# Performance work log

Measured on AMD Instinct MI355X. Metric: run time of the kernel, lower is better.

Reference implementation:

```python
import jax, jax.numpy as jnp
import numpy as np

B, L, V, E, H, S = 64, 128, 100000, 300, 400, 50
HD = H // 2
START_IDX, END_IDX = S - 2, S - 1


def setup_inputs():
    key = jax.random.key(0)
    ks = jax.random.split(key, 10)
    words = jax.random.randint(ks[0], (B, L), 0, V)
    word_seq_lens = jnp.full((B,), L, dtype=jnp.int32)
    masks = jnp.ones((B, L), dtype=bool)
    tags = jax.random.randint(ks[1], (B, L), 0, S - 2)
    emb_table = jax.random.normal(ks[2], (V, E), dtype=jnp.float32) * 0.1
    lw = lambda k, shp: jax.random.normal(k, shp, dtype=jnp.float32) * 0.05
    w_ih_f = lw(ks[3], (4 * HD, E)); w_hh_f = lw(ks[4], (4 * HD, HD)); b_f = jnp.zeros((4 * HD,), jnp.float32)
    w_ih_b = lw(ks[5], (4 * HD, E)); w_hh_b = lw(ks[6], (4 * HD, HD)); b_b = jnp.zeros((4 * HD,), jnp.float32)
    W_tag = lw(ks[7], (S, H)); b_tag = jnp.zeros((S,), jnp.float32)
    transition = jax.random.normal(ks[8], (S, S), dtype=jnp.float32)
    transition = transition.at[:, START_IDX].set(-10000.0).at[END_IDX, :].set(-10000.0)
    return dict(words=words, word_seq_lens=word_seq_lens, masks=masks, tags=tags,
                emb_table=emb_table, w_ih_f=w_ih_f, w_hh_f=w_hh_f, b_f=b_f,
                w_ih_b=w_ih_b, w_hh_b=w_hh_b, b_b=b_b, W_tag=W_tag, b_tag=b_tag,
                transition=transition)


def _lstm_dir(x, w_ih, w_hh, b, reverse):
    # x: (B, L, D) -> (B, L, HD). PyTorch gate order: i, f, g, o.
    bsz = x.shape[0]
    xg = jnp.einsum('bld,gd->blg', x, w_ih) + b  # precompute input projections

    def step(carry, xt):
        h, c = carry
        g = xt + h @ w_hh.T
        i, f, gg, o = jnp.split(g, 4, axis=-1)
        c = jax.nn.sigmoid(f) * c + jax.nn.sigmoid(i) * jnp.tanh(gg)
        h = jax.nn.sigmoid(o) * jnp.tanh(c)
        return (h, c), h

    init = (jnp.zeros((bsz, HD), x.dtype), jnp.zeros((bsz, HD), x.dtype))
    _, hs = jax.lax.scan(step, init, jnp.swapaxes(xg, 0, 1), reverse=reverse)
    return jnp.swapaxes(hs, 0, 1)


def _forward_nll(words, word_seq_lens, masks, tags, emb_table,
                 w_ih_f, w_hh_f, b_f, w_ih_b, w_hh_b, b_b, W_tag, b_tag, transition):
    word_emb = emb_table[words]                              # (B, L, E); dropout = identity (eval)
    h_f = _lstm_dir(word_emb, w_ih_f, w_hh_f, b_f, reverse=False)
    h_b = _lstm_dir(word_emb, w_ih_b, w_hh_b, b_b, reverse=True)
    lstm_out = jnp.concatenate([h_f, h_b], axis=-1)          # (B, L, H)
    features = jnp.einsum('blh,sh->bls', lstm_out, W_tag) + b_tag  # (B, L, S)
    # all_scores[b,t,prev,cur] = transition[prev,cur] + features[b,t,cur]
    all_scores = transition[None, None] + features[:, :, None, :]  # (B, L, S, S)

    # ---- forward algorithm (unlabeled partition) ----
    alpha0 = all_scores[:, 0, START_IDX, :]                   # (B, S)

    def step(alpha, scores_t):
        alpha = jax.nn.logsumexp(alpha[:, :, None] + scores_t, axis=1)
        return alpha, alpha

    _, alphas_rest = jax.lax.scan(step, alpha0, jnp.swapaxes(all_scores[:, 1:], 0, 1))
    alphas = jnp.concatenate([alpha0[None], alphas_rest], axis=0)  # (L, B, S)
    alphas = jnp.swapaxes(alphas, 0, 1)                            # (B, L, S)
    last_alpha = jnp.take_along_axis(alphas, (word_seq_lens - 1)[:, None, None], axis=1)[:, 0]
    last_alpha = last_alpha + transition[:, END_IDX][None]
    unlabeled = jnp.sum(jax.nn.logsumexp(last_alpha, axis=1))

    # ---- gold path score (labeled) ----
    cur = jnp.take_along_axis(
        all_scores, jnp.broadcast_to(tags[:, :, None, None], (B, L, S, 1)), axis=3)[..., 0]  # (B, L, S)
    mid = jnp.take_along_axis(cur[:, 1:], tags[:, :L - 1, None], axis=2)[..., 0]             # (B, L-1)
    begin = cur[:, 0, START_IDX]
    end_tag_ids = jnp.take_along_axis(tags, (word_seq_lens - 1)[:, None], axis=1)[:, 0]
    end = transition[end_tag_ids, END_IDX]
    labeled = jnp.sum(begin) + jnp.sum(jnp.where(masks[:, 1:], mid, 0.0)) + jnp.sum(end)

    return unlabeled - labeled


def reference(words, word_seq_lens, masks, tags, emb_table, w_ih_f, w_hh_f, b_f,
              w_ih_b, w_hh_b, b_b, W_tag, b_tag, transition):
    return _forward_nll(words, word_seq_lens, masks, tags, emb_table,
                        w_ih_f, w_hh_f, b_f, w_ih_b, w_hh_b, b_b,
                        W_tag, b_tag, transition)
```

## Files before the change

kernel.cpp:

```cpp
#include <hip/hip_runtime.h>
#include <hip/hip_fp16.h>

#define B_ 64
#define L_ 128
#define E_ 300
#define HD_ 200
#define H_ 400
#define S_ 50
#define START_ 48
#define END_ 49
#define NG_ 1600
#define BL_ 8192

#define OFF_XG   0ull
#define OFF_LSTM 26214400ull
#define OFF_ABF  OFF_LSTM
#define OFF_BBF  (OFF_LSTM + 5242880ull)
#define OFF_SH   (OFF_LSTM + 13107200ull)
#define OFF_INV  (OFF_SH + 1638400ull)
#define OFF_WTB  (OFF_INV + 6400ull)
#define OFF_BIA  (OFF_WTB + 80000ull)
#define OFF_PART (OFF_BIA + 6400ull)

#define NA_T 2621440
#define NB_T 532480
#define PREP_BLOCKS 12427

typedef __attribute__((ext_vector_type(8))) short short8;
typedef __attribute__((ext_vector_type(4))) float f32x4;

__device__ __forceinline__ unsigned short f32_to_bf16(float f) {
    unsigned u = __float_as_uint(f);
    unsigned r = u + 0x7fffu + ((u >> 16) & 1u);
    return (unsigned short)(r >> 16);
}
__device__ __forceinline__ float bf16_to_f32(unsigned short s) {
    return __uint_as_float(((unsigned)s) << 16);
}
__device__ __forceinline__ int dot4(unsigned a, unsigned b, int c) {
#if __has_builtin(__builtin_amdgcn_sdot4)
    return __builtin_amdgcn_sdot4(a, b, c, false);
#else
    c += (int)(signed char)(a)       * (int)(signed char)(b);
    c += (int)(signed char)(a >> 8)  * (int)(signed char)(b >> 8);
    c += (int)(signed char)(a >> 16) * (int)(signed char)(b >> 16);
    c += (int)(signed char)(a >> 24) * (int)(signed char)(b >> 24);
    return c;
#endif
}
__device__ __forceinline__ float rlanef(float v, int l) {
#if __has_builtin(__builtin_amdgcn_readlane)
    return __uint_as_float(__builtin_amdgcn_readlane(__float_as_uint(v), l));
#else
    return __shfl(v, l, 64);
#endif
}

__global__ void prep_kernel(const int* __restrict__ words, const float* __restrict__ emb,
                            const float* __restrict__ wihf, const float* __restrict__ wihb,
                            const float* __restrict__ bfc, const float* __restrict__ bbc,
                            const float* __restrict__ wtag,
                            unsigned short* __restrict__ Abf, unsigned short* __restrict__ Bbf,
                            unsigned short* __restrict__ wtagB, float* __restrict__ biasC) {
    long g = (long)blockIdx.x * 256 + threadIdx.x;
    if (g < NA_T) {
        int i = (int)(g / 320), k = (int)(g % 320);
        float v = (k < E_) ? emb[(long)words[i] * E_ + k] : 0.f;
        Abf[g] = f32_to_bf16(v);
        return;
    }
    g -= NA_T;
    if (g < NB_T) {
        int r = (int)(g / 320), k = (int)(g % 320);
        float v = 0.f;
        if (r < NG_ && k < E_) v = (r < 800) ? wihf[r * E_ + k] : wihb[(r - 800) * E_ + k];
        Bbf[g] = f32_to_bf16(v);
        return;
    }
    g -= NB_T;
    if (g < 25600) {
        int s = (int)(g / 400), k = (int)(g % 400);
        float v = (s < S_) ? wtag[s * H_ + k] : 0.f;
        wtagB[g] = f32_to_bf16(v);
        return;
    }
    g -= 25600;
    if (g < 1600) { biasC[g] = (g < 800) ? bfc[g] : bbc[g - 800]; return; }
}

__global__ __launch_bounds__(256) void quant_kernel(const float* __restrict__ whh_f,
                                                    const float* __restrict__ whh_b,
                                                    signed char* __restrict__ w8,
                                                    float* __restrict__ invs) {
    int gw = (int)((blockIdx.x * 256 + threadIdx.x) >> 6);
    int lane = threadIdx.x & 63;
    if (gw >= 1600) return;
    int dir = gw / 800, row = gw % 800;
    const float* w = (dir ? whh_b : whh_f) + row * HD_;
    float m = 1e-20f;
    for (int k = lane; k < HD_; k += 64) m = fmaxf(m, fabsf(w[k]));
    for (int off = 32; off; off >>= 1) m = fmaxf(m, __shfl_xor(m, off));
    float s = 127.f / m;
    if (lane < 50) {
        int k0 = lane * 4;
        unsigned pk = 0;
#pragma unroll
        for (int i = 0; i < 4; ++i) {
            int v = (int)rintf(w[k0 + i] * s);
            pk |= ((unsigned)(v & 0xff)) << (8 * i);
        }
        unsigned char* base = (unsigned char*)w8 + dir * 160000;
        if (lane < 48) {
            int j = lane >> 2, wsel = lane & 3;
            *(unsigned*)(base + (size_t)(j * 800 + row) * 16 + wsel * 4) = pk;
        } else {
            *(unsigned*)(base + 153600 + (size_t)row * 8 + (lane - 48) * 4) = pk;
        }
    }
    if (lane == 0) invs[gw] = m / 16129.f;
}

__global__ __launch_bounds__(256) void xg_gemm(const unsigned short* __restrict__ Abf,
                                               const unsigned short* __restrict__ Bbf,
                                               const float* __restrict__ biasC,
                                               unsigned short* __restrict__ xg) {
    __shared__ unsigned short As[128 * 40];
    __shared__ unsigned short Bs[128 * 40];
    int tid = threadIdx.x;
    int bm = blockIdx.y * 128;
    int bn = blockIdx.x * 128;
    int srow = tid >> 1, half = tid & 1;
    int lane = tid & 63, wave = tid >> 6, r16 = lane & 15, kh = lane >> 4;

    f32x4 acc[2][8];
#pragma unroll
    for (int mi = 0; mi < 2; ++mi)
#pragma unroll
        for (int ni = 0; ni < 8; ++ni) acc[mi][ni] = (f32x4){0.f, 0.f, 0.f, 0.f};

    const unsigned short* Ar = Abf + (long)(bm + srow) * 320;
    const unsigned short* Br = Bbf + (long)(bn + srow) * 320;

    for (int k0 = 0; k0 < 320; k0 += 32) {
#pragma unroll
        for (int j = 0; j < 2; ++j) {
            int off = half * 16 + j * 8;
            *(uint4*)&As[srow * 40 + off] = *(const uint4*)(Ar + k0 + off);
            *(uint4*)&Bs[srow * 40 + off] = *(const uint4*)(Br + k0 + off);
        }
        __syncthreads();
        short8 af[2], bfv[8];
#pragma unroll
        for (int mi = 0; mi < 2; ++mi)
            af[mi] = *(const short8*)&As[(wave * 32 + mi * 16 + r16) * 40 + kh * 8];
#pragma unroll
        for (int ni = 0; ni < 8; ++ni)
            bfv[ni] = *(const short8*)&Bs[(ni * 16 + r16) * 40 + kh * 8];
#pragma unroll
        for (int mi = 0; mi < 2; ++mi)
#pragma unroll
            for (int ni = 0; ni < 8; ++ni)
                acc[mi][ni] = __builtin_amdgcn_mfma_f32_16x16x32_bf16(af[mi], bfv[ni], acc[mi][ni], 0, 0, 0);
        __syncthreads();
    }
#pragma unroll
    for (int ni = 0; ni < 8; ++ni) {
        int g = bn + ni * 16 + r16;
        if (g < NG_) {
            float bias = biasC[g];
#pragma unroll
            for (int mi = 0; mi < 2; ++mi) {
#pragma unroll
                for (int r = 0; r < 4; ++r) {
                    int row = bm + wave * 32 + mi * 16 + kh * 4 + r;
                    xg[(long)row * NG_ + g] = f32_to_bf16(acc[mi][ni][r] + bias);
                }
            }
        }
    }
}

__global__ __launch_bounds__(832) void lstm_rec(const unsigned short* __restrict__ xg,
                                                const signed char* __restrict__ w8,
                                                const float* __restrict__ invs,
                                                unsigned short* __restrict__ lstm16) {
    __shared__ __align__(16) unsigned char hbuf[256];
    __shared__ float a_lds[800];
    int tid = threadIdx.x;
    int dir = blockIdx.x >> 6;
    int b = blockIdx.x & 63;
    bool act = tid < 800;
    int tw = act ? tid : 0;
    int q = tid / 200;

    const unsigned char* wbase = (const unsigned char*)w8 + dir * 160000;
    uint4 wA[12];
    uint2 wAt;
#pragma unroll
    for (int j = 0; j < 12; ++j)
        wA[j] = *(const uint4*)(wbase + (size_t)(j * 800 + tw) * 16);
    wAt = *(const uint2*)(wbase + 153600 + (size_t)tw * 8);
#pragma unroll
    for (int j = 0; j < 12; ++j)
        asm volatile("" : "+v"(wA[j].x), "+v"(wA[j].y), "+v"(wA[j].z), "+v"(wA[j].w));
    asm volatile("" : "+v"(wAt.x), "+v"(wAt.y));

    float invsc = act ? invs[dir * 800 + tid] : 0.f;
    if (tid < 64) ((unsigned*)hbuf)[tid] = 0u;
    float c = 0.f;
    __syncthreads();

    const uint4* h4c = (const uint4*)hbuf;
    const uint2* ht2 = (const uint2*)(hbuf + 192);
    const unsigned short* xbase = xg + (long)b * L_ * NG_ + dir * 800;

    int t0 = dir ? (L_ - 1) : 0;
    float x = act ? bf16_to_f32(xbase[(long)t0 * NG_ + tid]) : 0.f;

    for (int step = 0; step < L_; ++step) {
        int t = dir ? (L_ - 1 - step) : step;
        float x_n = 0.f;
        if (act && step + 1 < L_) {
            int tn = dir ? (t - 1) : (t + 1);
            x_n = bf16_to_f32(xbase[(long)tn * NG_ + tid]);
        }
        if (act) {
            int di = 0;
#pragma unroll
            for (int j = 0; j < 12; ++j) {
                uint4 hh = h4c[j];
                di = dot4(wA[j].x, hh.x, di); di = dot4(wA[j].y, hh.y, di);
                di = dot4(wA[j].z, hh.z, di); di = dot4(wA[j].w, hh.w, di);
            }
            {
                uint2 hh = ht2[0];
                di = dot4(wAt.x, hh.x, di); di = dot4(wAt.y, hh.y, di);
            }
            float p = x + (float)di * invsc;
            float av;
            if (q == 2) {
                float e = __expf(-2.f * p);
                av = 2.f / (1.f + e) - 1.f;
            } else {
                av = 1.f / (1.f + __expf(-p));
            }
            a_lds[tid] = av;
        }
        __syncthreads();
        if (tid < HD_) {
            float ig = a_lds[tid];
            float fg = a_lds[200 + tid];
            float gg = a_lds[400 + tid];
            float og = a_lds[600 + tid];
            c = fg * c + ig * gg;
            float ec = __expf(-2.f * c);
            float hn = og * (2.f / (1.f + ec) - 1.f);
            ((signed char*)hbuf)[tid] = (signed char)(int)rintf(hn * 127.f);
            lstm16[((long)(b * L_ + t)) * H_ + dir * HD_ + tid] = f32_to_bf16(hn);
        }
        x = x_n;
        __syncthreads();
    }
}

__global__ __launch_bounds__(256) void feat_kernel(const unsigned short* __restrict__ lstm16,
                                                   const unsigned short* __restrict__ wtagB,
                                                   const float* __restrict__ btag,
                                                   float* __restrict__ feats) {
    __shared__ unsigned short As[128 * 40];
    __shared__ unsigned short Bs[64 * 40];
    int tid = threadIdx.x;
    int bm = blockIdx.x * 128;
    int srow = tid >> 1, half = tid & 1;
    int lane = tid & 63, wave = tid >> 6, r16 = lane & 15, kh = lane >> 4;

    f32x4 acc[2][4];
#pragma unroll
    for (int mi = 0; mi < 2; ++mi)
#pragma unroll
        for (int ni = 0; ni < 4; ++ni) acc[mi][ni] = (f32x4){0.f, 0.f, 0.f, 0.f};

    const unsigned short* Ar = lstm16 + (long)(bm + srow) * 400;
    const unsigned short* Br = wtagB + (long)srow * 400;

    for (int k0 = 0; k0 < 400; k0 += 32) {
#pragma unroll
        for (int j = 0; j < 2; ++j) {
            int off = half * 16 + j * 8;
            bool kv = (k0 + off + 8 <= 400);
            uint4 z = make_uint4(0u, 0u, 0u, 0u);
            *(uint4*)&As[srow * 40 + off] = kv ? *(const uint4*)(Ar + k0 + off) : z;
            if (srow < 64)
                *(uint4*)&Bs[srow * 40 + off] = kv ? *(const uint4*)(Br + k0 + off) : z;
        }
        __syncthreads();
        short8 af[2], bfv[4];
#pragma unroll
        for (int mi = 0; mi < 2; ++mi)
            af[mi] = *(const short8*)&As[(wave * 32 + mi * 16 + r16) * 40 + kh * 8];
#pragma unroll
        for (int ni = 0; ni < 4; ++ni)
            bfv[ni] = *(const short8*)&Bs[(ni * 16 + r16) * 40 + kh * 8];
#pragma unroll
        for (int mi = 0; mi < 2; ++mi)
#pragma unroll
            for (int ni = 0; ni < 4; ++ni)
                acc[mi][ni] = __builtin_amdgcn_mfma_f32_16x16x32_bf16(af[mi], bfv[ni], acc[mi][ni], 0, 0, 0);
        __syncthreads();
    }
#pragma unroll
    for (int ni = 0; ni < 4; ++ni) {
        int g = ni * 16 + r16;
        if (g < S_) {
            float bias = btag[g];
#pragma unroll
            for (int mi = 0; mi < 2; ++mi) {
#pragma unroll
                for (int r = 0; r < 4; ++r) {
                    int row = bm + wave * 32 + mi * 16 + kh * 4 + r;
                    feats[(long)row * S_ + g] = acc[mi][ni][r] + bias;
                }
            }
        }
    }
}

__global__ __launch_bounds__(64) void crf_kernel(const float* __restrict__ feats,
                                                 const float* __restrict__ trans,
                                                 const int* __restrict__ tags,
                                                 const int* __restrict__ seqlens,
                                                 float* __restrict__ part) {
    __shared__ float Tt[S_ * 53];
    __shared__ int tg[L_];
    int lane = threadIdx.x;
    int b = blockIdx.x;
    for (int idx = lane; idx < S_ * S_; idx += 64) {
        int j = idx / S_, i = idx % S_;
        Tt[j * 53 + i] = trans[i * S_ + j];
    }
    for (int idx = lane; idx < L_; idx += 64) tg[idx] = tags[b * L_ + idx];
    int slen = seqlens[b];
    const float* fb = feats + (long)b * L_ * S_;
    __syncthreads();

    bool act = lane < S_;
    const float* Trow = Tt + (act ? lane : 0) * 53;
    float eT[S_];
#pragma unroll
    for (int i = 0; i < S_; ++i) eT[i] = __expf(Trow[i]);

    float alpha = act ? (Trow[START_] + fb[lane]) : -1e30f;
    float lal = alpha;
    float fval = act ? fb[S_ + lane] : 0.f;

    for (int t = 1; t < L_; ++t) {
        float fval_n = (act && t + 1 < L_) ? fb[(t + 1) * S_ + lane] : 0.f;
        float m = alpha;
        for (int off = 32; off; off >>= 1) m = fmaxf(m, __shfl_xor(m, off));
        float p = __expf(alpha - m);
        float s0 = 0.f, s1 = 0.f, s2 = 0.f, s3 = 0.f, s4 = 0.f;
#pragma unroll
        for (int i = 0; i < S_; i += 5) {
            s0 = fmaf(rlanef(p, i),     eT[i],     s0);
            s1 = fmaf(rlanef(p, i + 1), eT[i + 1], s1);
            s2 = fmaf(rlanef(p, i + 2), eT[i + 2], s2);
            s3 = fmaf(rlanef(p, i + 3), eT[i + 3], s3);
            s4 = fmaf(rlanef(p, i + 4), eT[i + 4], s4);
        }
        float s = fmaxf(((s0 + s1) + (s2 + s3)) + s4, 1e-38f);
        float anew = m + __logf(s) + fval;
        alpha = act ? anew : -1e30f;
        if (t == slen - 1) lal = alpha;
        fval = fval_n;
    }

    float la = act ? (lal + Tt[END_ * 53 + lane]) : -1e30f;
    float m = la;
    for (int off = 32; off; off >>= 1) m = fmaxf(m, __shfl_xor(m, off));
    float e = act ? __expf(la - m) : 0.f;
    for (int off = 32; off; off >>= 1) e += __shfl_xor(e, off);
    float unl = m + __logf(e);

    float lab = 0.f;
    for (int tt = lane; tt < L_; tt += 64) {
        if (tt == 0) {
            lab += Tt[tg[0] * 53 + START_] + fb[tg[0]];
        } else if (tt < slen) {
            lab += Tt[tg[tt] * 53 + tg[tt - 1]] + fb[tt * S_ + tg[tt]];
        }
    }
    if (lane == 0) lab += Tt[END_ * 53 + tg[slen - 1]];
    for (int off = 32; off; off >>= 1) lab += __shfl_xor(lab, off);
    if (lane == 0) part[b] = unl - lab;
}

__global__ void fin_kernel(const float* __restrict__ part, float* __restrict__ out) {
    float s = 0.f;
    for (int i = 0; i < B_; ++i) s += part[i];
    out[0] = s;
}

extern "C" void kernel_launch(void* const* d_in, const int* in_sizes, int n_in,
                              void* d_out, int out_size, void* d_ws, size_t ws_size,
                              hipStream_t stream) {
    const int*   words = (const int*)d_in[0];
    const int*   slens = (const int*)d_in[1];
    const int*   tags  = (const int*)d_in[3];
    const float* emb   = (const float*)d_in[4];
    const float* wihf  = (const float*)d_in[5];
    const float* whhf  = (const float*)d_in[6];
    const float* bf    = (const float*)d_in[7];
    const float* wihb  = (const float*)d_in[8];
    const float* whhb  = (const float*)d_in[9];
    const float* bb    = (const float*)d_in[10];
    const float* wtag  = (const float*)d_in[11];
    const float* btag  = (const float*)d_in[12];
    const float* trans = (const float*)d_in[13];

    char* ws = (char*)d_ws;
    unsigned short* xg     = (unsigned short*)(ws + OFF_XG);
    unsigned short* lstm16 = (unsigned short*)(ws + OFF_LSTM);
    unsigned short* Abf    = (unsigned short*)(ws + OFF_ABF);
    unsigned short* Bbf    = (unsigned short*)(ws + OFF_BBF);
    signed char*    w8     = (signed char*)(ws + OFF_SH);
    float*          fts    = (float*)(ws + OFF_SH);
    float*          invs   = (float*)(ws + OFF_INV);
    unsigned short* wtagB  = (unsigned short*)(ws + OFF_WTB);
    float*          biaC   = (float*)(ws + OFF_BIA);
    float*          part   = (float*)(ws + OFF_PART);
    float*          out    = (float*)d_out;

    prep_kernel<<<PREP_BLOCKS, 256, 0, stream>>>(words, emb, wihf, wihb, bf, bb,
                                                 wtag, Abf, Bbf, wtagB, biaC);
    quant_kernel<<<400, 256, 0, stream>>>(whhf, whhb, w8, invs);
    xg_gemm<<<dim3(13, 64), 256, 0, stream>>>(Abf, Bbf, biaC, xg);
    lstm_rec<<<128, 832, 0, stream>>>(xg, w8, invs, lstm16);
    feat_kernel<<<64, 256, 0, stream>>>(lstm16, wtagB, btag, fts);
    crf_kernel<<<64, 64, 0, stream>>>(fts, trans, tags, slens, part);
    fin_kernel<<<1, 1, 0, stream>>>(part, out);
}
```

Before: 263.6 us.

## Quantize recurrent LSTM weights to 4-bit packed nibbles held in registers

The recurrent weight matrix is now quantized to signed 4-bit values (scale 7) instead of int8, with two nibbles per byte, and each thread keeps 25 32-bit registers instead of 50. In the inner loop, shifts and masks place the nibbles in the high bits of each byte so the existing int8 dot4 can be used, and the hidden-state byte layout is permuted to match. The goal is lower register pressure and less weight loading in the sequential recurrence kernel, in exchange for extra ALU work per dot product and a much coarser weight precision that may break numerical accuracy.

```diff
diff --git a/kernel.cpp b/kernel.cpp
--- a/kernel.cpp
+++ b/kernel.cpp
@@ -90,7 +90,7 @@
 
 __global__ __launch_bounds__(256) void quant_kernel(const float* __restrict__ whh_f,
                                                     const float* __restrict__ whh_b,
-                                                    signed char* __restrict__ w8,
+                                                    unsigned* __restrict__ w4g,
                                                     float* __restrict__ invs) {
     int gw = (int)((blockIdx.x * 256 + threadIdx.x) >> 6);
     int lane = threadIdx.x & 63;
@@ -100,24 +100,20 @@
     float m = 1e-20f;
     for (int k = lane; k < HD_; k += 64) m = fmaxf(m, fabsf(w[k]));
     for (int off = 32; off; off >>= 1) m = fmaxf(m, __shfl_xor(m, off));
-    float s = 127.f / m;
-    if (lane < 50) {
-        int k0 = lane * 4;
-        unsigned pk = 0;
-#pragma unroll
-        for (int i = 0; i < 4; ++i) {
-            int v = (int)rintf(w[k0 + i] * s);
-            pk |= ((unsigned)(v & 0xff)) << (8 * i);
-        }
-        unsigned char* base = (unsigned char*)w8 + dir * 160000;
-        if (lane < 48) {
-            int j = lane >> 2, wsel = lane & 3;
-            *(unsigned*)(base + (size_t)(j * 800 + row) * 16 + wsel * 4) = pk;
-        } else {
-            *(unsigned*)(base + 153600 + (size_t)row * 8 + (lane - 48) * 4) = pk;
-        }
-    }
-    if (lane == 0) invs[gw] = m / 16129.f;
+    float s4 = 7.f / m;
+    if (lane < 25) {
+        int k0 = lane * 8;
+        unsigned word = 0;
+#pragma unroll
+        for (int b1 = 0; b1 < 4; ++b1) {
+            int ne = (int)rintf(w[k0 + 2 * b1] * s4);
+            int no = (int)rintf(w[k0 + 2 * b1 + 1] * s4);
+            word |= ((unsigned)(ne & 0xF)) << (8 * b1);
+            word |= ((unsigned)(no & 0xF)) << (8 * b1 + 4);
+        }
+        w4g[(size_t)dir * 20000 + lane * 800 + row] = word;
+    }
+    if (lane == 0) invs[gw] = m / 14224.f;
 }
 
 __global__ __launch_bounds__(256) void xg_gemm(const unsigned short* __restrict__ Abf,
@@ -181,7 +177,7 @@
 }
 
 __global__ __launch_bounds__(832) void lstm_rec(const unsigned short* __restrict__ xg,
-                                                const signed char* __restrict__ w8,
+                                                const unsigned* __restrict__ w4g,
                                                 const float* __restrict__ invs,
                                                 unsigned short* __restrict__ lstm16) {
     __shared__ __align__(16) unsigned char hbuf[256];
@@ -193,17 +189,12 @@
     int tw = act ? tid : 0;
     int q = tid / 200;
 
-    const unsigned char* wbase = (const unsigned char*)w8 + dir * 160000;
-    uint4 wA[12];
-    uint2 wAt;
-#pragma unroll
-    for (int j = 0; j < 12; ++j)
-        wA[j] = *(const uint4*)(wbase + (size_t)(j * 800 + tw) * 16);
-    wAt = *(const uint2*)(wbase + 153600 + (size_t)tw * 8);
-#pragma unroll
-    for (int j = 0; j < 12; ++j)
-        asm volatile("" : "+v"(wA[j].x), "+v"(wA[j].y), "+v"(wA[j].z), "+v"(wA[j].w));
-    asm volatile("" : "+v"(wAt.x), "+v"(wAt.y));
+    const unsigned* wptr = w4g + (size_t)dir * 20000;
+    unsigned w25[25];
+#pragma unroll
+    for (int j = 0; j < 25; ++j) w25[j] = wptr[j * 800 + tw];
+#pragma unroll
+    for (int j = 0; j < 25; ++j) asm volatile("" : "+v"(w25[j]));
 
     float invsc = act ? invs[dir * 800 + tid] : 0.f;
     if (tid < 64) ((unsigned*)hbuf)[tid] = 0u;
@@ -216,6 +207,7 @@
 
     int t0 = dir ? (L_ - 1) : 0;
     float x = act ? bf16_to_f32(xbase[(long)t0 * NG_ + tid]) : 0.f;
+    const unsigned M = 0xF0F0F0F0u;
 
     for (int step = 0; step < L_; ++step) {
         int t = dir ? (L_ - 1 - step) : step;
@@ -227,14 +219,19 @@
         if (act) {
             int di = 0;
 #pragma unroll
-            for (int j = 0; j < 12; ++j) {
-                uint4 hh = h4c[j];
-                di = dot4(wA[j].x, hh.x, di); di = dot4(wA[j].y, hh.y, di);
-                di = dot4(wA[j].z, hh.z, di); di = dot4(wA[j].w, hh.w, di);
+            for (int jj = 0; jj < 12; ++jj) {
+                uint4 hh = h4c[jj];
+                unsigned w0 = w25[2 * jj], w1 = w25[2 * jj + 1];
+                di = dot4((w0 << 4) & M, hh.x, di);
+                di = dot4(w0 & M,        hh.y, di);
+                di = dot4((w1 << 4) & M, hh.z, di);
+                di = dot4(w1 & M,        hh.w, di);
             }
             {
                 uint2 hh = ht2[0];
-                di = dot4(wAt.x, hh.x, di); di = dot4(wAt.y, hh.y, di);
+                unsigned w0 = w25[24];
+                di = dot4((w0 << 4) & M, hh.x, di);
+                di = dot4(w0 & M,        hh.y, di);
             }
             float p = x + (float)di * invsc;
             float av;
@@ -255,7 +252,9 @@
             c = fg * c + ig * gg;
             float ec = __expf(-2.f * c);
             float hn = og * (2.f / (1.f + ec) - 1.f);
-            ((signed char*)hbuf)[tid] = (signed char)(int)rintf(hn * 127.f);
+            int jj = tid >> 3, r = tid & 7;
+            ((signed char*)hbuf)[jj * 8 + (r & 1) * 4 + (r >> 1)] =
+                (signed char)(int)rintf(hn * 127.f);
             lstm16[((long)(b * L_ + t)) * H_ + dir * HD_ + tid] = f32_to_bf16(hn);
         }
         x = x_n;
@@ -422,7 +421,7 @@
     unsigned short* lstm16 = (unsigned short*)(ws + OFF_LSTM);
     unsigned short* Abf    = (unsigned short*)(ws + OFF_ABF);
     unsigned short* Bbf    = (unsigned short*)(ws + OFF_BBF);
-    signed char*    w8     = (signed char*)(ws + OFF_SH);
+    unsigned*       w4g    = (unsigned*)(ws + OFF_SH);
     float*          fts    = (float*)(ws + OFF_SH);
     float*          invs   = (float*)(ws + OFF_INV);
     unsigned short* wtagB  = (unsigned short*)(ws + OFF_WTB);
@@ -432,9 +431,9 @@
 
     prep_kernel<<<PREP_BLOCKS, 256, 0, stream>>>(words, emb, wihf, wihb, bf, bb,
                                                  wtag, Abf, Bbf, wtagB, biaC);
-    quant_kernel<<<400, 256, 0, stream>>>(whhf, whhb, w8, invs);
+    quant_kernel<<<400, 256, 0, stream>>>(whhf, whhb, w4g, invs);
     xg_gemm<<<dim3(13, 64), 256, 0, stream>>>(Abf, Bbf, biaC, xg);
-    lstm_rec<<<128, 832, 0, stream>>>(xg, w8, invs, lstm16);
+    lstm_rec<<<128, 832, 0, stream>>>(xg, w4g, invs, lstm16);
     feat_kernel<<<64, 256, 0, stream>>>(lstm16, wtagB, btag, fts);
     crf_kernel<<<64, 64, 0, stream>>>(fts, trans, tags, slens, part);
     fin_kernel<<<1, 1, 0, stream>>>(part, out);
```

New measurement: 264.2 us. Within noise of the previous version (+0.2%).
